# Performance work log

Hardware: AMD Instinct MI355X
Metric: run time of the kernel (lower is better)

Reference implementation:

```python
import jax, jax.numpy as jnp
import numpy as np

BETA = 0.25          # commitment loss weight (init kwarg)
CODEBOOK_SIZE = 2048


def setup_inputs() -> dict:
    key = jax.random.key(0)
    k1, k2 = jax.random.split(key)
    B, L, D = 8, 4096, 256
    z_e = jax.random.normal(k1, (B, L, D), dtype=jnp.float32)
    # xavier_uniform-style init for the codebook
    limit = float(np.sqrt(6.0 / (CODEBOOK_SIZE + D)))
    embed_weight = jax.random.uniform(k2, (CODEBOOK_SIZE, D), dtype=jnp.float32,
                                      minval=-limit, maxval=limit)
    return {"z_e": z_e, "embed_weight": embed_weight}


def reference(z_e, embed_weight):
    # eval-mode forward (no EMA buffer updates)
    B, L, D = z_e.shape
    K = embed_weight.shape[0]
    zf = z_e.reshape(-1, D)                                   # [N, D]
    d2 = (jnp.sum(zf * zf, axis=1, keepdims=True)
          - 2.0 * (zf @ embed_weight.T)
          + jnp.sum(embed_weight * embed_weight, axis=1)[None, :])
    distances = jnp.sqrt(jnp.maximum(d2, 0.0))                # [N, K]
    idx = jnp.argmin(distances, axis=1)                       # [N]
    z_q = embed_weight[idx].reshape(B, L, D)                  # gather

    commitment_loss = BETA * jnp.mean((jax.lax.stop_gradient(z_q) - z_e) ** 2)
    embedding_loss = jnp.mean((jax.lax.stop_gradient(z_e) - z_q) ** 2)

    # avg over one-hot encodings == normalized histogram of idx
    N = zf.shape[0]
    counts = jax.ops.segment_sum(jnp.ones((N,), jnp.float32), idx, num_segments=K)
    avg_probs = counts / N
    perplexity = jnp.exp(-jnp.sum(avg_probs * jnp.log(avg_probs + 1e-10)))
    vq_loss = commitment_loss + embedding_loss - 0.01 * perplexity

    z_q_st = z_e + jax.lax.stop_gradient(z_q - z_e)           # straight-through
    return z_q_st, vq_loss, idx.reshape(B, L)
```

## Files before the change

### kernel.cpp

```cpp
#include <hip/hip_runtime.h>
#include <math.h>

#define DDIM 256
#define NSPLIT 4
#define TILES_PER_SPLIT 16
#define TILE_CODES 32
#define TILE_BYTES 16384
#define ROWS_PER_BLOCK 128

typedef __attribute__((ext_vector_type(8))) short short8v;
typedef __attribute__((ext_vector_type(4))) float float4v;
typedef unsigned int u32;
typedef unsigned short u16;

__device__ __forceinline__ short f2bf(float x) {
    u32 u = __float_as_uint(x);
    u = u + 0x7fffu + ((u >> 16) & 1u);
    return (short)(u >> 16);
}

__device__ __forceinline__ void gload_lds16(const void* g, void* l) {
    __builtin_amdgcn_global_load_lds(
        (const __attribute__((address_space(1))) u32*)g,
        (__attribute__((address_space(3))) u32*)l, 16, 0, 0);
}

__device__ __forceinline__ float np_sq_chain(const float* v, int lane) {
    #pragma clang fp contract(off)
    const int half = lane >> 3, j = lane & 7;
    const float* base = v + half * 128 + j;
    float x = base[0];
    float c = x * x;
    #pragma unroll
    for (int m = 1; m < 16; ++m) {
        float y = base[8 * m];
        float s = y * y;
        c = c + s;
    }
    return c;
}

__device__ __forceinline__ float np_combine16(const float* c) {
    #pragma clang fp contract(off)
    float L = ((c[0] + c[1]) + (c[2] + c[3])) + ((c[4] + c[5]) + (c[6] + c[7]));
    float R = ((c[8] + c[9]) + (c[10] + c[11])) + ((c[12] + c[13]) + (c[14] + c[15]));
    return L + R;
}

__device__ __forceinline__ void ins3(float m, int k,
                                     float& v0, float& v1, float& v2,
                                     int& i0, int& i1, int& i2) {
    if (m < v0)      { v2 = v1; i2 = i1; v1 = v0; i1 = i0; v0 = m; i0 = k; }
    else if (m < v1) { v2 = v1; i2 = i1; v1 = m;  i1 = k; }
    else if (m < v2) { v2 = m;  i2 = k; }
}

__global__ void zero_counts_kernel(int* __restrict__ counts, int K) {
    int i = blockIdx.x * 256 + threadIdx.x;
    if (i < K) counts[i] = 0;
}

__global__ void code_norms_np_kernel(const float* __restrict__ e, float* __restrict__ e2) {
    __shared__ float buf[DDIM];
    __shared__ float ch[16];
    int k = blockIdx.x;
    int t = threadIdx.x;
    float4 v = *(const float4*)&e[(size_t)k * DDIM + t * 4];
    *(float4*)&buf[t * 4] = v;
    __syncthreads();
    if (t < 16) ch[t] = np_sq_chain(buf, t);
    __syncthreads();
    if (t == 0) e2[k] = np_combine16(ch);
}

__global__ void convert_permute_e_kernel(const float* __restrict__ e, char* __restrict__ ebf_p) {
    int id = blockIdx.x * 256 + threadIdx.x;
    int k = id >> 5, d8 = id & 31;
    const float* s = &e[(size_t)k * DDIM + d8 * 8];
    float4 f0 = *(const float4*)s;
    float4 f1 = *(const float4*)(s + 4);
    short8v v;
    v[0] = f2bf(f0.x); v[1] = f2bf(f0.y); v[2] = f2bf(f0.z); v[3] = f2bf(f0.w);
    v[4] = f2bf(f1.x); v[5] = f2bf(f1.y); v[6] = f2bf(f1.z); v[7] = f2bf(f1.w);
    *(short8v*)(ebf_p + ((size_t)(k >> 5) << 14) + d8 * 512 + (k & 31) * 16) = v;
}

__global__ __attribute__((amdgpu_flat_work_group_size(512, 512)))
__attribute__((amdgpu_waves_per_eu(8, 8)))
void vq_cand_kernel(const float* __restrict__ z, const char* __restrict__ ebf_p,
                    const float* __restrict__ e2, float* __restrict__ cand_v,
                    u16* __restrict__ cand_i, int N) {
    __shared__ __align__(16) char smem[2][TILE_BYTES];
    __shared__ float e2s[512];
    const int t    = threadIdx.x;
    const int w    = t >> 6;
    const int lane = t & 63;
    const int quad = lane >> 4;
    const int l15  = lane & 15;
    const int s    = blockIdx.y;
    const int row0 = blockIdx.x * ROWS_PER_BLOCK;
    const int rw   = row0 + w * 16;

    const char* tile_base = ebf_p + (size_t)s * TILES_PER_SPLIT * TILE_BYTES;

    {
        const char* src = tile_base + t * 16;
        char* dst = (char*)smem[0] + t * 16;
        gload_lds16(src,                     dst);
        gload_lds16(src + 8192,              dst + 8192);
        gload_lds16(src + TILE_BYTES,        dst + TILE_BYTES);
        gload_lds16(src + TILE_BYTES + 8192, dst + TILE_BYTES + 8192);
    }

    e2s[t] = e2[s * 512 + t];

    short8v zf[8];
    {
        const float* zr = &z[(size_t)(rw + l15) * DDIM];
        #pragma unroll
        for (int kk = 0; kk < 8; ++kk) {
            int d0 = kk * 32 + quad * 8;
            float4 f0 = *(const float4*)&zr[d0];
            float4 f1 = *(const float4*)&zr[d0 + 4];
            short8v v;
            v[0] = f2bf(f0.x); v[1] = f2bf(f0.y); v[2] = f2bf(f0.z); v[3] = f2bf(f0.w);
            v[4] = f2bf(f1.x); v[5] = f2bf(f1.y); v[6] = f2bf(f1.z); v[7] = f2bf(f1.w);
            zf[kk] = v;
        }
    }

    float v0 = 3.4e38f, v1 = 3.4e38f, v2 = 3.4e38f;
    int   i0 = 0x7fff,  i1 = 0x7fff,  i2 = 0x7fff;

    asm volatile("s_waitcnt lgkmcnt(0)" ::: "memory");
    __builtin_amdgcn_s_barrier();

    #pragma unroll 1
    for (int tt = 0; tt < TILES_PER_SPLIT; ++tt) {
        if (tt < TILES_PER_SPLIT - 1)
            asm volatile("s_waitcnt vmcnt(2)" ::: "memory");
        else
            asm volatile("s_waitcnt vmcnt(0)" ::: "memory");
        __builtin_amdgcn_s_barrier();

        const char* es = smem[tt & 1];
        const int kloc  = tt * TILE_CODES;
        const int kbase = s * 512 + kloc;
        float4 e2a = *(const float4*)&e2s[kloc + quad * 4];
        float4 e2b = *(const float4*)&e2s[kloc + 16 + quad * 4];

        float4v acc0 = (float4v)0.0f, acc1 = (float4v)0.0f;

        #pragma unroll
        for (int kk = 0; kk < 8; ++kk) {
            int c = kk * 4 + quad;
            short8v a0 = *(const short8v*)(es + c * 512 + l15 * 16);
            short8v a1 = *(const short8v*)(es + c * 512 + (16 + l15) * 16);
            acc0 = __builtin_amdgcn_mfma_f32_16x16x32_bf16(a0, zf[kk], acc0, 0, 0, 0);
            acc1 = __builtin_amdgcn_mfma_f32_16x16x32_bf16(a1, zf[kk], acc1, 0, 0, 0);
        }

        float m;
        m = fmaf(-2.0f, acc0[0], e2a.x); ins3(m, kbase + quad * 4 + 0,      v0, v1, v2, i0, i1, i2);
        m = fmaf(-2.0f, acc1[0], e2b.x); ins3(m, kbase + 16 + quad * 4 + 0, v0, v1, v2, i0, i1, i2);
        m = fmaf(-2.0f, acc0[1], e2a.y); ins3(m, kbase + quad * 4 + 1,      v0, v1, v2, i0, i1, i2);
        m = fmaf(-2.0f, acc1[1], e2b.y); ins3(m, kbase + 16 + quad * 4 + 1, v0, v1, v2, i0, i1, i2);
        m = fmaf(-2.0f, acc0[2], e2a.z); ins3(m, kbase + quad * 4 + 2,      v0, v1, v2, i0, i1, i2);
        m = fmaf(-2.0f, acc1[2], e2b.z); ins3(m, kbase + 16 + quad * 4 + 2, v0, v1, v2, i0, i1, i2);
        m = fmaf(-2.0f, acc0[3], e2a.w); ins3(m, kbase + quad * 4 + 3,      v0, v1, v2, i0, i1, i2);
        m = fmaf(-2.0f, acc1[3], e2b.w); ins3(m, kbase + 16 + quad * 4 + 3, v0, v1, v2, i0, i1, i2);

        asm volatile("s_waitcnt lgkmcnt(0)" ::: "memory");
        __builtin_amdgcn_s_barrier();

        if (tt + 2 < TILES_PER_SPLIT) {
            const char* src = tile_base + (size_t)(tt + 2) * TILE_BYTES + t * 16;
            char* dst = (char*)smem[tt & 1] + t * 16;
            gload_lds16(src,        dst);
            gload_lds16(src + 8192, dst + 8192);
        }
    }

    {
        float bm0 = 3.4e38f, bm1 = 3.4e38f, bm2 = 3.4e38f;
        int   bk0 = 0x7fff,  bk1 = 0x7fff,  bk2 = 0x7fff;
        #pragma unroll
        for (int q = 0; q < 4; ++q) {
            int src = l15 + q * 16;
            float m0 = __shfl(v0, src); int k0 = __shfl(i0, src);
            float m1 = __shfl(v1, src); int k1 = __shfl(i1, src);
            float m2 = __shfl(v2, src); int k2 = __shfl(i2, src);
            ins3(m0, k0, bm0, bm1, bm2, bk0, bk1, bk2);
            ins3(m1, k1, bm0, bm1, bm2, bk0, bk1, bk2);
            ins3(m2, k2, bm0, bm1, bm2, bk0, bk1, bk2);
        }
        if (quad == 0) {
            size_t base = ((size_t)s * N + (rw + l15)) * 3;
            cand_v[base]     = bm0;  cand_i[base]     = (u16)bk0;
            cand_v[base + 1] = bm1;  cand_i[base + 1] = (u16)bk1;
            cand_v[base + 2] = bm2;  cand_i[base + 2] = (u16)bk2;
        }
    }
}

__global__ void refine_fused_kernel(const float* __restrict__ z, const float* __restrict__ e,
                                    const float* __restrict__ e2np,
                                    const float* __restrict__ cand_v,
                                    const u16* __restrict__ cand_i,
                                    int* __restrict__ counts, float* __restrict__ partials,
                                    float* __restrict__ out_zq, float* __restrict__ out_idx,
                                    int N) {
    __shared__ float buf[4][DDIM];
    __shared__ float ch[4][16];
    __shared__ float wsum[4];
    const int w = threadIdx.x >> 6;
    const int t = threadIdx.x & 63;
    const int n = blockIdx.x * 4 + w;

    float4 zv = *(const float4*)&z[(size_t)n * DDIM + t * 4];
    *(float4*)&buf[w][t * 4] = zv;
    __syncthreads();
    if (t < 16) ch[w][t] = np_sq_chain(buf[w], t);
    __syncthreads();

    float bv[6]; int bi[6];
    #pragma unroll
    for (int c = 0; c < 6; ++c) { bv[c] = 3.4e38f; bi[c] = 0x7fffffff; }
    #pragma unroll
    for (int c = 0; c < 12; ++c) {
        int sp = c / 3, j = c - sp * 3;
        size_t off = ((size_t)sp * N + n) * 3 + j;
        float v  = cand_v[off];
        int   id = (int)cand_i[off];
        #pragma unroll
        for (int x = 0; x < 6; ++x) {
            if (v < bv[x] || (v == bv[x] && id < bi[x])) {
                for (int d = 5; d > x; --d) { bv[d] = bv[d - 1]; bi[d] = bi[d - 1]; }
                bv[x] = v; bi[x] = id;
                break;
            }
        }
    }

    float dotf[6];
    #pragma unroll
    for (int c = 0; c < 6; ++c) {
        int k = bi[c];
        float4 ev = *(const float4*)&e[(size_t)k * DDIM + t * 4];
        double p = (double)zv.x * (double)ev.x + (double)zv.y * (double)ev.y
                 + (double)zv.z * (double)ev.z + (double)zv.w * (double)ev.w;
        #pragma unroll
        for (int o = 32; o > 0; o >>= 1) p += __shfl_down(p, o);
        dotf[c] = (float)p;
    }

    int bk = 0;
    if (t == 0) {
        #pragma clang fp contract(off)
        float sx = np_combine16(ch[w]);
        float bd = 3.4e38f;
        bk = 0x7fffffff;
        #pragma unroll
        for (int c = 0; c < 6; ++c) {
            float twod = 2.0f * dotf[c];
            float t1 = sx - twod;
            float d2v = t1 + e2np[bi[c]];
            d2v = fmaxf(d2v, 0.0f);
            float d = sqrtf(d2v);
            if (d < bd || (d == bd && bi[c] < bk)) { bd = d; bk = bi[c]; }
        }
    }
    int wk = __shfl(bk, 0);

    float4 ev = *(const float4*)&e[(size_t)wk * DDIM + t * 4];
    *(float4*)&out_zq[(size_t)n * DDIM + t * 4] = ev;
    float dx = zv.x - ev.x, dy = zv.y - ev.y, dz = zv.z - ev.z, dw = zv.w - ev.w;
    float sq = dx * dx + dy * dy + dz * dz + dw * dw;
    #pragma unroll
    for (int o = 32; o > 0; o >>= 1) sq += __shfl_down(sq, o);
    if (t == 0) {
        wsum[w] = sq;
        atomicAdd(&counts[wk], 1);
        out_idx[n] = (float)wk;
    }
    __syncthreads();
    if (threadIdx.x == 0)
        partials[blockIdx.x] = wsum[0] + wsum[1] + wsum[2] + wsum[3];
}

__global__ void finalize_kernel(const int* __restrict__ counts, const float* __restrict__ partials,
                                float* __restrict__ out_loss, int K, int NB,
                                float invN, float invND) {
    int t = threadIdx.x;
    double ent = 0.0, sq = 0.0;
    for (int k = t; k < K; k += 256) {
        float p = (float)counts[k] * invN;
        ent += (double)(p * logf(p + 1e-10f));
    }
    for (int i = t; i < NB; i += 256) sq += (double)partials[i];
    #pragma unroll
    for (int o = 32; o > 0; o >>= 1) {
        ent += __shfl_down(ent, o);
        sq  += __shfl_down(sq, o);
    }
    __shared__ double e4[4], s4[4];
    if ((t & 63) == 0) { e4[t >> 6] = ent; s4[t >> 6] = sq; }
    __syncthreads();
    if (t == 0) {
        double esum = e4[0] + e4[1] + e4[2] + e4[3];
        double ssum = s4[0] + s4[1] + s4[2] + s4[3];
        float perp = expf((float)(-esum));
        float mean = (float)ssum * invND;
        out_loss[0] = 1.25f * mean - 0.01f * perp;
    }
}

extern "C" void kernel_launch(void* const* d_in, const int* in_sizes, int n_in,
                              void* d_out, int out_size, void* d_ws, size_t ws_size,
                              hipStream_t stream) {
    const float* z = (const float*)d_in[0];
    const float* e = (const float*)d_in[1];
    const int N = in_sizes[0] / DDIM;
    const int K = in_sizes[1] / DDIM;

    float* out      = (float*)d_out;
    float* out_zq   = out;
    float* out_loss = out + (size_t)N * DDIM;
    float* out_idx  = out_loss + 1;

    int*   counts   = (int*)d_ws;
    float* e2np     = (float*)((char*)d_ws + 8192);
    float* partials = (float*)((char*)d_ws + 16384);
    float* cand_v   = (float*)((char*)d_ws + 49152);
    u16*   cand_i   = (u16*)((char*)d_ws + 1622016);
    char*  ebf_p    = (char*)d_ws + 2408448;

    zero_counts_kernel<<<(K + 255) / 256, 256, 0, stream>>>(counts, K);
    code_norms_np_kernel<<<K, 64, 0, stream>>>(e, e2np);
    convert_permute_e_kernel<<<K * 32 / 256, 256, 0, stream>>>(e, ebf_p);
    vq_cand_kernel<<<dim3(N / ROWS_PER_BLOCK, NSPLIT), 512, 0, stream>>>(z, ebf_p, e2np,
                                                                         cand_v, cand_i, N);
    refine_fused_kernel<<<N / 4, 256, 0, stream>>>(z, e, e2np, cand_v, cand_i,
                                                   counts, partials, out_zq, out_idx, N);
    finalize_kernel<<<1, 256, 0, stream>>>(counts, partials, out_loss, K, N / 4,
                                           1.0f / (float)N, 1.0f / (float)(N * DDIM));
}
```

Baseline: 450.9 us.

## Stage z fragments in LDS and shrink vq_cand blocks to 256 threads

The candidate-search kernel now uses 64-row, 256-thread blocks, with each wave loading 4 KB of every codebook tile into LDS via four global_load_lds ops instead of two. The bf16 z fragments are moved from registers into per-wave LDS, so each MFMA step reloads its z operand from LDS. This cuts VGPR pressure and drops the fixed waves_per_eu setting, so more, smaller blocks can be resident. The cost is extra LDS traffic per tile, more LDS per block (56 KB), and twice as many blocks re-reading the codebook.

```diff
diff --git a/kernel.cpp b/kernel.cpp
--- a/kernel.cpp
+++ b/kernel.cpp
@@ -6,7 +6,7 @@
 #define TILES_PER_SPLIT 16
 #define TILE_CODES 32
 #define TILE_BYTES 16384
-#define ROWS_PER_BLOCK 128
+#define ROWS_PER_BLOCK 64
 
 typedef __attribute__((ext_vector_type(8))) short short8v;
 typedef __attribute__((ext_vector_type(4))) float float4v;
@@ -85,12 +85,12 @@
     *(short8v*)(ebf_p + ((size_t)(k >> 5) << 14) + d8 * 512 + (k & 31) * 16) = v;
 }
 
-__global__ __attribute__((amdgpu_flat_work_group_size(512, 512)))
-__attribute__((amdgpu_waves_per_eu(8, 8)))
+__global__ __attribute__((amdgpu_flat_work_group_size(256, 256)))
 void vq_cand_kernel(const float* __restrict__ z, const char* __restrict__ ebf_p,
                     const float* __restrict__ e2, float* __restrict__ cand_v,
                     u16* __restrict__ cand_i, int N) {
     __shared__ __align__(16) char smem[2][TILE_BYTES];
+    __shared__ __align__(16) char zlds[4][8192];
     __shared__ float e2s[512];
     const int t    = threadIdx.x;
     const int w    = t >> 6;
@@ -98,34 +98,35 @@
     const int quad = lane >> 4;
     const int l15  = lane & 15;
     const int s    = blockIdx.y;
-    const int row0 = blockIdx.x * ROWS_PER_BLOCK;
-    const int rw   = row0 + w * 16;
+    const int rw0  = blockIdx.x * ROWS_PER_BLOCK + w * 16;
 
     const char* tile_base = ebf_p + (size_t)s * TILES_PER_SPLIT * TILE_BYTES;
 
     {
-        const char* src = tile_base + t * 16;
-        char* dst = (char*)smem[0] + t * 16;
-        gload_lds16(src,                     dst);
-        gload_lds16(src + 8192,              dst + 8192);
-        gload_lds16(src + TILE_BYTES,        dst + TILE_BYTES);
-        gload_lds16(src + TILE_BYTES + 8192, dst + TILE_BYTES + 8192);
-    }
-
-    e2s[t] = e2[s * 512 + t];
-
-    short8v zf[8];
+        const char* src0 = tile_base + w * 4096 + lane * 16;
+        char* dst0 = smem[0] + w * 4096;
+        char* dst1 = smem[1] + w * 4096;
+        #pragma unroll
+        for (int q = 0; q < 4; ++q) gload_lds16(src0 + q * 1024, dst0 + q * 1024);
+        #pragma unroll
+        for (int q = 0; q < 4; ++q) gload_lds16(src0 + TILE_BYTES + q * 1024, dst1 + q * 1024);
+    }
+
+    e2s[t]       = e2[s * 512 + t];
+    e2s[t + 256] = e2[s * 512 + t + 256];
+
     {
-        const float* zr = &z[(size_t)(rw + l15) * DDIM];
-        #pragma unroll
-        for (int kk = 0; kk < 8; ++kk) {
-            int d0 = kk * 32 + quad * 8;
-            float4 f0 = *(const float4*)&zr[d0];
-            float4 f1 = *(const float4*)&zr[d0 + 4];
+        char* zw = zlds[w];
+        const float* zr = &z[(size_t)(rw0 + l15) * DDIM];
+        #pragma unroll
+        for (int c2 = 0; c2 < 8; ++c2) {
+            int c = c2 * 4 + quad;
+            float4 f0 = *(const float4*)&zr[c * 8];
+            float4 f1 = *(const float4*)&zr[c * 8 + 4];
             short8v v;
             v[0] = f2bf(f0.x); v[1] = f2bf(f0.y); v[2] = f2bf(f0.z); v[3] = f2bf(f0.w);
             v[4] = f2bf(f1.x); v[5] = f2bf(f1.y); v[6] = f2bf(f1.z); v[7] = f2bf(f1.w);
-            zf[kk] = v;
+            *(short8v*)(zw + c * 256 + l15 * 16) = v;
         }
     }
 
@@ -133,12 +134,13 @@
     int   i0 = 0x7fff,  i1 = 0x7fff,  i2 = 0x7fff;
 
     asm volatile("s_waitcnt lgkmcnt(0)" ::: "memory");
-    __builtin_amdgcn_s_barrier();
+
+    const char* zw = zlds[w];
 
     #pragma unroll 1
     for (int tt = 0; tt < TILES_PER_SPLIT; ++tt) {
         if (tt < TILES_PER_SPLIT - 1)
-            asm volatile("s_waitcnt vmcnt(2)" ::: "memory");
+            asm volatile("s_waitcnt vmcnt(4)" ::: "memory");
         else
             asm volatile("s_waitcnt vmcnt(0)" ::: "memory");
         __builtin_amdgcn_s_barrier();
@@ -156,8 +158,9 @@
             int c = kk * 4 + quad;
             short8v a0 = *(const short8v*)(es + c * 512 + l15 * 16);
             short8v a1 = *(const short8v*)(es + c * 512 + (16 + l15) * 16);
-            acc0 = __builtin_amdgcn_mfma_f32_16x16x32_bf16(a0, zf[kk], acc0, 0, 0, 0);
-            acc1 = __builtin_amdgcn_mfma_f32_16x16x32_bf16(a1, zf[kk], acc1, 0, 0, 0);
+            short8v zb = *(const short8v*)(zw + c * 256 + l15 * 16);
+            acc0 = __builtin_amdgcn_mfma_f32_16x16x32_bf16(a0, zb, acc0, 0, 0, 0);
+            acc1 = __builtin_amdgcn_mfma_f32_16x16x32_bf16(a1, zb, acc1, 0, 0, 0);
         }
 
         float m;
@@ -174,10 +177,10 @@
         __builtin_amdgcn_s_barrier();
 
         if (tt + 2 < TILES_PER_SPLIT) {
-            const char* src = tile_base + (size_t)(tt + 2) * TILE_BYTES + t * 16;
-            char* dst = (char*)smem[tt & 1] + t * 16;
-            gload_lds16(src,        dst);
-            gload_lds16(src + 8192, dst + 8192);
+            const char* src = tile_base + (size_t)(tt + 2) * TILE_BYTES + w * 4096 + lane * 16;
+            char* dst = smem[tt & 1] + w * 4096;
+            #pragma unroll
+            for (int q = 0; q < 4; ++q) gload_lds16(src + q * 1024, dst + q * 1024);
         }
     }
 
@@ -195,7 +198,7 @@
             ins3(m2, k2, bm0, bm1, bm2, bk0, bk1, bk2);
         }
         if (quad == 0) {
-            size_t base = ((size_t)s * N + (rw + l15)) * 3;
+            size_t base = ((size_t)s * N + (rw0 + l15)) * 3;
             cand_v[base]     = bm0;  cand_i[base]     = (u16)bk0;
             cand_v[base + 1] = bm1;  cand_i[base + 1] = (u16)bk1;
             cand_v[base + 2] = bm2;  cand_i[base + 2] = (u16)bk2;
@@ -338,7 +341,7 @@
     zero_counts_kernel<<<(K + 255) / 256, 256, 0, stream>>>(counts, K);
     code_norms_np_kernel<<<K, 64, 0, stream>>>(e, e2np);
     convert_permute_e_kernel<<<K * 32 / 256, 256, 0, stream>>>(e, ebf_p);
-    vq_cand_kernel<<<dim3(N / ROWS_PER_BLOCK, NSPLIT), 512, 0, stream>>>(z, ebf_p, e2np,
+    vq_cand_kernel<<<dim3(N / ROWS_PER_BLOCK, NSPLIT), 256, 0, stream>>>(z, ebf_p, e2np,
                                                                          cand_v, cand_i, N);
     refine_fused_kernel<<<N / 4, 256, 0, stream>>>(z, e, e2np, cand_v, cand_i,
                                                    counts, partials, out_zq, out_idx, N);
```

Result: slower. 568.7 us (+26.1%).
